# Kernel optimization log

Measured on AMD Instinct MI355X. Metric: run time of the kernel, lower is better.

The kernel has to match this reference:

```python
import jax, jax.numpy as jnp
import numpy as np

B, T, C, H, HS, L, V, BITS = 4, 512, 768, 12, 64, 12, 50257, 16


def _ln(x, g, b, eps=1e-5):
    m = x.mean(-1, keepdims=True)
    v = ((x - m) ** 2).mean(-1, keepdims=True)
    return (x - m) * jax.lax.rsqrt(v + eps) * g + b


def setup_inputs() -> dict:
    key = jax.random.key(0)
    ks = jax.random.split(key, 12)
    s = 0.02
    return {
        "idx": jax.random.randint(ks[0], (B, T), 0, V),
        "tok_emb": jax.random.normal(ks[1], (V, C), jnp.float32) * s,
        "pos_emb": jax.random.normal(ks[2], (T, C), jnp.float32) * s,
        "Wq": jax.random.normal(ks[3], (L, H, C, HS), jnp.float32) * s,
        "Wk": jax.random.normal(ks[4], (L, H, C, HS), jnp.float32) * s,
        "Wv": jax.random.normal(ks[5], (L, H, C, HS), jnp.float32) * s,
        "Wo": jax.random.normal(ks[6], (L, C, C), jnp.float32) * s,
        "bo": jnp.zeros((L, C), jnp.float32),
        "W1": jax.random.normal(ks[7], (L, C, 4 * C), jnp.float32) * s,
        "b1": jnp.zeros((L, 4 * C), jnp.float32),
        "W2": jax.random.normal(ks[8], (L, 4 * C, C), jnp.float32) * s,
        "b2": jnp.zeros((L, C), jnp.float32),
        "ln1_g": jnp.ones((L, C), jnp.float32),
        "ln1_b": jnp.zeros((L, C), jnp.float32),
        "ln2_g": jnp.ones((L, C), jnp.float32),
        "ln2_b": jnp.zeros((L, C), jnp.float32),
        "lnf_g": jnp.ones((C,), jnp.float32),
        "lnf_b": jnp.zeros((C,), jnp.float32),
        "Wh": jax.random.normal(ks[9], (C, BITS), jnp.float32) * s,
        "bh": jnp.zeros((BITS,), jnp.float32),
    }


def reference(idx, tok_emb, pos_emb, Wq, Wk, Wv, Wo, bo, W1, b1, W2, b2,
              ln1_g, ln1_b, ln2_g, ln2_b, lnf_g, lnf_b, Wh, bh):
    Bc, Tc = idx.shape
    x = tok_emb[idx] + pos_emb[:Tc]          # [B,T,C]
    mask = jnp.tril(jnp.ones((Tc, Tc), bool))  # causal tril buffer
    scale = HS ** -0.5

    def block(x, p):
        wq, wk, wv, wo, bo_, w1, b1_, w2, b2_, g1, bb1, g2, bb2 = p
        xn = _ln(x, g1, bb1)
        q = jnp.einsum('btc,hcd->bhtd', xn, wq)
        k = jnp.einsum('btc,hcd->bhtd', xn, wk)
        v = jnp.einsum('btc,hcd->bhtd', xn, wv)
        wei = jnp.einsum('bhtd,bhsd->bhts', q, k) * scale
        wei = jnp.where(mask, wei, -jnp.inf)
        wei = jax.nn.softmax(wei, axis=-1)
        o = jnp.einsum('bhts,bhsd->bhtd', wei, v)
        o = o.transpose(0, 2, 1, 3).reshape(Bc, Tc, H * HS)  # concat heads
        x = x + o @ wo + bo_
        xn2 = _ln(x, g2, bb2)
        h = jax.nn.gelu(xn2 @ w1 + b1_, approximate=False)  # exact GELU (torch default)
        x = x + h @ w2 + b2_
        return x, None

    x, _ = jax.lax.scan(block, x, (Wq, Wk, Wv, Wo, bo, W1, b1, W2, b2,
                                   ln1_g, ln1_b, ln2_g, ln2_b))
    x = _ln(x, lnf_g, lnf_b)
    logits = x @ Wh + bh                      # [B,T,16] ECOC logits
    return logits
```

## Files before the change

### kernel.cpp

```cpp
#include <hip/hip_runtime.h>
#include <hip/hip_bf16.h>
#include <math.h>

#define TT   512
#define CC   768
#define HH   12
#define HSZ  64
#define LL   12
#define C4   3072
#define BTOT 2048
#define NQKV 2304
#define NX   ((long)BTOT * CC)

typedef __attribute__((ext_vector_type(8))) short short8;
typedef __attribute__((ext_vector_type(4))) float f32x4;

__device__ __forceinline__ unsigned short f2b_bits(float f) {
    unsigned u = __float_as_uint(f);
    return (unsigned short)((u + 0x7fffu + ((u >> 16) & 1u)) >> 16);
}
__device__ __forceinline__ float b2f(unsigned short b) {
    return __uint_as_float((unsigned)b << 16);
}
__device__ __forceinline__ float gelu_t(float v) {
    float u = 0.7978845608f * fmaf(0.044715f * v, v * v, v);
    float th = 1.f - 2.f / (1.f + __expf(2.f * u));
    return 0.5f * v * (1.f + th);
}

__device__ __forceinline__ void gl_lds16(const void* g, void* l) {
    __builtin_amdgcn_global_load_lds(
        (const __attribute__((address_space(1))) unsigned int*)g,
        (__attribute__((address_space(3))) unsigned int*)l,
        16, 0, 0);
}

__global__ __launch_bounds__(256) void embed_ln(const int* __restrict__ idx,
    const float* __restrict__ tok, const float* __restrict__ pos,
    const float* __restrict__ g, const float* __restrict__ b,
    float* __restrict__ x, __hip_bfloat16* __restrict__ y)
{
    int r = blockIdx.x, tid = threadIdx.x;
    int t = r & (TT - 1);
    long id = idx[r];
    const float* te = tok + id * (long)CC;
    const float* pe = pos + (long)t * CC;
    float* xr = x + (long)r * CC;
    float v[3];
#pragma unroll
    for (int i = 0; i < 3; ++i) {
        int c = tid + i * 256;
        v[i] = te[c] + pe[c];
        xr[c] = v[i];
    }
    float s  = v[0] + v[1] + v[2];
    float sq = v[0]*v[0] + v[1]*v[1] + v[2]*v[2];
#pragma unroll
    for (int off = 32; off > 0; off >>= 1) {
        s  += __shfl_down(s, off);
        sq += __shfl_down(sq, off);
    }
    __shared__ float ss[4], ssq[4];
    int w = tid >> 6;
    if ((tid & 63) == 0) { ss[w] = s; ssq[w] = sq; }
    __syncthreads();
    s  = ss[0] + ss[1] + ss[2] + ss[3];
    sq = ssq[0] + ssq[1] + ssq[2] + ssq[3];
    float mean = s * (1.0f / CC);
    float var  = sq * (1.0f / CC) - mean * mean;
    float rs   = rsqrtf(var + 1e-5f);
    __hip_bfloat16* yr = y + (long)r * CC;
#pragma unroll
    for (int i = 0; i < 3; ++i) {
        int c = tid + i * 256;
        yr[c] = __float2bfloat16((v[i] - mean) * rs * g[c] + b[c]);
    }
}

template <bool DOLN>
__global__ __launch_bounds__(256) void red_ln(float* __restrict__ x,
    const unsigned short* __restrict__ p, const float* __restrict__ bias,
    const float* __restrict__ g, const float* __restrict__ b,
    __hip_bfloat16* __restrict__ y)
{
    int r = blockIdx.x, tid = threadIdx.x;
    float* xr = x + (long)r * CC;
    const unsigned short* pr = p + (long)r * CC;
    float v[3];
#pragma unroll
    for (int i = 0; i < 3; ++i) {
        int c = tid + i * 256;
        float s = xr[c] + bias[c];
        s += b2f(pr[c]);
        s += b2f(pr[c + 1 * NX]);
        s += b2f(pr[c + 2 * NX]);
        s += b2f(pr[c + 3 * NX]);
        xr[c] = s;
        v[i] = s;
    }
    if (!DOLN) return;
    float s  = v[0] + v[1] + v[2];
    float sq = v[0]*v[0] + v[1]*v[1] + v[2]*v[2];
#pragma unroll
    for (int off = 32; off > 0; off >>= 1) {
        s  += __shfl_down(s, off);
        sq += __shfl_down(sq, off);
    }
    __shared__ float ss[4], ssq[4];
    int w = tid >> 6;
    if ((tid & 63) == 0) { ss[w] = s; ssq[w] = sq; }
    __syncthreads();
    s  = ss[0] + ss[1] + ss[2] + ss[3];
    sq = ssq[0] + ssq[1] + ssq[2] + ssq[3];
    float mean = s * (1.0f / CC);
    float var  = sq * (1.0f / CC) - mean * mean;
    float rs   = rsqrtf(var + 1e-5f);
    __hip_bfloat16* yr = y + (long)r * CC;
#pragma unroll
    for (int i = 0; i < 3; ++i) {
        int c = tid + i * 256;
        yr[c] = __float2bfloat16((v[i] - mean) * rs * g[c] + b[c]);
    }
}

__global__ __launch_bounds__(256) void cvtT_k(const float* __restrict__ src,
    __hip_bfloat16* __restrict__ dst, int R, int D, long sSrc, long sDst)
{
    src += (long)blockIdx.z * sSrc;
    dst += (long)blockIdx.z * sDst;
    __shared__ float t[64][65];
    int d0 = blockIdx.x * 64, r0 = blockIdx.y * 64;
    int tid = threadIdx.x;
#pragma unroll
    for (int i = 0; i < 4; ++i) {
        int flat = tid + i * 256;
        int r = flat >> 4, c4 = (flat & 15) * 4;
        float4 v = *(const float4*)&src[(long)(r0 + r) * D + d0 + c4];
        t[r][c4 + 0] = v.x; t[r][c4 + 1] = v.y;
        t[r][c4 + 2] = v.z; t[r][c4 + 3] = v.w;
    }
    __syncthreads();
#pragma unroll
    for (int i = 0; i < 4; ++i) {
        int flat = tid + i * 256;
        int n = flat >> 4, kq = (flat & 15) * 4;
        ushort4 o;
        o.x = f2b_bits(t[kq + 0][n]); o.y = f2b_bits(t[kq + 1][n]);
        o.z = f2b_bits(t[kq + 2][n]); o.w = f2b_bits(t[kq + 3][n]);
        *(ushort4*)&dst[(long)(d0 + n) * R + r0 + kq] = o;
    }
}

__global__ __launch_bounds__(256) void cvt_qkvT(const float* __restrict__ Wq,
    const float* __restrict__ Wk, const float* __restrict__ Wv,
    __hip_bfloat16* __restrict__ out)
{
    int c0 = blockIdx.x * 64;
    int g  = blockIdx.y;
    int l  = blockIdx.z;
    int which = g / 12, h = g % 12;
    const long wAtt = (long)HH * CC * HSZ;
    const float* src = (which == 0 ? Wq : which == 1 ? Wk : Wv)
                       + l * wAtt + (long)h * CC * HSZ;
    __hip_bfloat16* dst = out + (long)l * NQKV * CC + (long)(which * CC + h * HSZ) * CC;
    __shared__ float t[64][65];
    int tid = threadIdx.x;
#pragma unroll
    for (int i = 0; i < 4; ++i) {
        int flat = tid + i * 256;
        int r = flat >> 4, c4 = (flat & 15) * 4;
        float4 v = *(const float4*)&src[(long)(c0 + r) * HSZ + c4];
        t[r][c4 + 0] = v.x; t[r][c4 + 1] = v.y;
        t[r][c4 + 2] = v.z; t[r][c4 + 3] = v.w;
    }
    __syncthreads();
#pragma unroll
    for (int i = 0; i < 4; ++i) {
        int flat = tid + i * 256;
        int n = flat >> 4, kq = (flat & 15) * 4;
        ushort4 o;
        o.x = f2b_bits(t[kq + 0][n]); o.y = f2b_bits(t[kq + 1][n]);
        o.z = f2b_bits(t[kq + 2][n]); o.w = f2b_bits(t[kq + 3][n]);
        *(ushort4*)&dst[(long)n * CC + c0 + kq] = o;
    }
}

template <int EPI>
__global__ __launch_bounds__(256, 3) void gemm_bf16(
    const __hip_bfloat16* __restrict__ A,
    const __hip_bfloat16* __restrict__ BT,
    __hip_bfloat16* __restrict__ Cb, float* __restrict__ Cf,
    const float* __restrict__ bias, __hip_bfloat16* __restrict__ Vt,
    int K, int lda, int ldb, int ldc)
{
    __shared__ short Asm[4][64 * 32];
    __shared__ short Bsm[4][128 * 32];
    const int tid  = threadIdx.x;
    const int lane = tid & 63;
    const int wid  = tid >> 6;
    const int wm = wid >> 1, wn = wid & 1;

    const int gx = gridDim.x;
    const int slice = gx * gridDim.y;
    int flat = blockIdx.y * gx + blockIdx.x;
    int swz  = (flat & 7) * (slice >> 3) + (flat >> 3);
    const int row0 = (swz / gx) * 64, col0 = (swz % gx) * 128;
    const int sk = (EPI == 5) ? blockIdx.z : 0;

    const int gr = tid >> 2;
    const int cb = ((tid & 3) + (tid >> 3)) & 3;
    const int gk = cb * 8;
    const __hip_bfloat16* Ap = A  + (long)(row0 + gr) * lda + sk * K + gk;
    const __hip_bfloat16* Bp = BT + (long)(col0 + gr) * ldb + sk * K + gk;
    const int lofs = wid * 512;

    f32x4 acc[2][4] = {};
    const int fr = lane & 15, g = lane >> 4;

    int offA[2], offB[4];
#pragma unroll
    for (int m = 0; m < 2; ++m) {
        int row = wm * 32 + m * 16 + fr;
        offA[m] = row * 32 + (((g - (row >> 1)) & 3) * 8);
    }
#pragma unroll
    for (int n = 0; n < 4; ++n) {
        int row = wn * 64 + n * 16 + fr;
        offB[n] = row * 32 + (((g - (row >> 1)) & 3) * 8);
    }

#define STAGE(buf)                                                          \
    do {                                                                    \
        gl_lds16(Ap, &Asm[buf][lofs]);                                      \
        gl_lds16(Bp, &Bsm[buf][lofs]);                                      \
        gl_lds16(Bp + (long)64 * ldb, &Bsm[buf][lofs + 64 * 32]);           \
        Ap += 32; Bp += 32;                                                 \
    } while (0)

    STAGE(0); STAGE(1); STAGE(2);

    const int nt = K >> 5;
    for (int t = 0; t < nt; ++t) {
        if (t < nt - 2)       asm volatile("s_waitcnt vmcnt(6)" ::: "memory");
        else if (t == nt - 2) asm volatile("s_waitcnt vmcnt(3)" ::: "memory");
        else                  asm volatile("s_waitcnt vmcnt(0)" ::: "memory");
        __builtin_amdgcn_s_barrier();
        __builtin_amdgcn_sched_barrier(0);
        if (t + 3 < nt) STAGE((t + 3) & 3);

        const int cur = t & 3;
        short8 af[2], bf[4];
#pragma unroll
        for (int m = 0; m < 2; ++m)
            af[m] = *(const short8*)&Asm[cur][offA[m]];
#pragma unroll
        for (int n = 0; n < 4; ++n)
            bf[n] = *(const short8*)&Bsm[cur][offB[n]];
#pragma unroll
        for (int m = 0; m < 2; ++m)
#pragma unroll
            for (int n = 0; n < 4; ++n)
                acc[m][n] = __builtin_amdgcn_mfma_f32_16x16x32_bf16(
                    af[m], bf[n], acc[m][n], 0, 0, 0);
    }
#undef STAGE

    const int fq = lane >> 4;
#pragma unroll
    for (int m = 0; m < 2; ++m) {
        int rbase = row0 + wm * 32 + m * 16 + fq * 4;
#pragma unroll
        for (int n = 0; n < 4; ++n) {
            int col = col0 + wn * 64 + n * 16 + fr;
            if (EPI == 1 && col >= 1536) {
                int hd = col - 1536;
                int b = rbase >> 9, t = rbase & (TT - 1);
                ushort4 o;
                o.x = f2b_bits(acc[m][n][0]); o.y = f2b_bits(acc[m][n][1]);
                o.z = f2b_bits(acc[m][n][2]); o.w = f2b_bits(acc[m][n][3]);
                *(ushort4*)&Vt[((long)(b * HH + (hd >> 6)) * HSZ + (hd & 63)) * TT + t] = o;
                continue;
            }
            float bv = (EPI == 2) ? bias[col] : 0.f;
#pragma unroll
            for (int j = 0; j < 4; ++j) {
                long row = rbase + j;
                float v = acc[m][n][j];
                if (EPI == 1) {
                    Cb[row * ldc + col] = __float2bfloat16(v);
                } else if (EPI == 2) {
                    Cb[row * ldc + col] = __float2bfloat16(gelu_t(v + bv));
                } else {
                    Cb[(long)sk * NX + row * ldc + col] = __float2bfloat16(v);
                }
            }
        }
    }
}

__global__ __launch_bounds__(64) void attn_mfma(
    const __hip_bfloat16* __restrict__ qkv,
    const __hip_bfloat16* __restrict__ vT,
    __hip_bfloat16* __restrict__ o)
{
    int flat = blockIdx.x + 16 * (blockIdx.y + 12 * blockIdx.z);
    int swz  = (flat & 7) * 96 + (flat >> 3);
    const int qt = swz & 15;
    const int h  = (swz >> 4) % 12;
    const int b  = swz / 192;
    const int lane = threadIdx.x;
    const int t0 = qt * 32;
    const int fr = lane & 15, g = lane >> 4;

    __shared__ unsigned short P_lds[2][32 * 40];
    __shared__ float corr_lds[2][32], l_lds[32];

    const long qbaseA = ((long)(b * TT + t0 + fr)) * NQKV + h * HSZ + g * 8;
    const long qbaseB = qbaseA + (long)16 * NQKV;
    short8 qfA0 = *(const short8*)(qkv + qbaseA);
    short8 qfA1 = *(const short8*)(qkv + qbaseA + 32);
    short8 qfB0 = *(const short8*)(qkv + qbaseB);
    short8 qfB1 = *(const short8*)(qkv + qbaseB + 32);

    f32x4 oaccA[4] = {}, oaccB[4] = {};
    float mA = -3.0e38f, lA = 0.f, mB = -3.0e38f, lB = 0.f;
    const int t_laneA = t0 + fr;
    const int t_laneB = t0 + 16 + fr;
    const int smax = t0 + 31;
    const long kcol = CC + h * HSZ + g * 8;
    const long vrow = (((long)(b * HH + h) * HSZ) + fr) * TT + g * 8;

    short8 ka0, ka1, ka2, ka3;
    {
        long kb0 = ((long)(b * TT + fr)) * NQKV + kcol;
        long kb1 = ((long)(b * TT + 16 + fr)) * NQKV + kcol;
        ka0 = *(const short8*)(qkv + kb0);
        ka1 = *(const short8*)(qkv + kb0 + 32);
        ka2 = *(const short8*)(qkv + kb1);
        ka3 = *(const short8*)(qkv + kb1 + 32);
    }

    for (int s0 = 0; s0 <= smax; s0 += 32) {
        const int pc = (s0 >> 5) & 1;
        f32x4 stA0 = {}, stA1 = {}, stB0 = {}, stB1 = {};
        stA0 = __builtin_amdgcn_mfma_f32_16x16x32_bf16(ka0, qfA0, stA0, 0, 0, 0);
        stA0 = __builtin_amdgcn_mfma_f32_16x16x32_bf16(ka1, qfA1, stA0, 0, 0, 0);
        stA1 = __builtin_amdgcn_mfma_f32_16x16x32_bf16(ka2, qfA0, stA1, 0, 0, 0);
        stA1 = __builtin_amdgcn_mfma_f32_16x16x32_bf16(ka3, qfA1, stA1, 0, 0, 0);
        stB0 = __builtin_amdgcn_mfma_f32_16x16x32_bf16(ka0, qfB0, stB0, 0, 0, 0);
        stB0 = __builtin_amdgcn_mfma_f32_16x16x32_bf16(ka1, qfB1, stB0, 0, 0, 0);
        stB1 = __builtin_amdgcn_mfma_f32_16x16x32_bf16(ka2, qfB0, stB1, 0, 0, 0);
        stB1 = __builtin_amdgcn_mfma_f32_16x16x32_bf16(ka3, qfB1, stB1, 0, 0, 0);

        const bool more = (s0 + 32 <= smax);
        short8 kn0, kn1, kn2, kn3;
        if (more) {
            long kb0 = ((long)(b * TT + s0 + 32 + fr)) * NQKV + kcol;
            long kb1 = ((long)(b * TT + s0 + 48 + fr)) * NQKV + kcol;
            kn0 = *(const short8*)(qkv + kb0);
            kn1 = *(const short8*)(qkv + kb0 + 32);
            kn2 = *(const short8*)(qkv + kb1);
            kn3 = *(const short8*)(qkv + kb1 + 32);
        }
        short8 vc0 = *(const short8*)(vT + vrow + s0);
        short8 vc1 = *(const short8*)(vT + vrow + 16 * TT + s0);
        short8 vc2 = *(const short8*)(vT + vrow + 32 * TT + s0);
        short8 vc3 = *(const short8*)(vT + vrow + 48 * TT + s0);

        float pA[8];
        float mxA = -3.0e38f;
#pragma unroll
        for (int j = 0; j < 4; ++j) {
            int s = s0 + g * 4 + j;
            float v = stA0[j] * 0.125f;
            v = (s <= t_laneA) ? v : -3.0e38f;
            pA[j] = v; mxA = fmaxf(mxA, v);
        }
#pragma unroll
        for (int j = 0; j < 4; ++j) {
            int s = s0 + 16 + g * 4 + j;
            float v = stA1[j] * 0.125f;
            v = (s <= t_laneA) ? v : -3.0e38f;
            pA[4 + j] = v; mxA = fmaxf(mxA, v);
        }
        mxA = fmaxf(mxA, __shfl_xor(mxA, 16));
        mxA = fmaxf(mxA, __shfl_xor(mxA, 32));
        float mnewA = fmaxf(mA, mxA);
        float corrA = __expf(mA - mnewA);
        float psA = 0.f;
#pragma unroll
        for (int i = 0; i < 8; ++i) {
            float e = __expf(pA[i] - mnewA);
            pA[i] = e; psA += e;
        }
        psA += __shfl_xor(psA, 16);
        psA += __shfl_xor(psA, 32);
        lA = lA * corrA + psA;
        mA = mnewA;

        float pB[8];
        float mxB = -3.0e38f;
#pragma unroll
        for (int j = 0; j < 4; ++j) {
            int s = s0 + g * 4 + j;
            float v = stB0[j] * 0.125f;
            v = (s <= t_laneB) ? v : -3.0e38f;
            pB[j] = v; mxB = fmaxf(mxB, v);
        }
#pragma unroll
        for (int j = 0; j < 4; ++j) {
            int s = s0 + 16 + g * 4 + j;
            float v = stB1[j] * 0.125f;
            v = (s <= t_laneB) ? v : -3.0e38f;
            pB[4 + j] = v; mxB = fmaxf(mxB, v);
        }
        mxB = fmaxf(mxB, __shfl_xor(mxB, 16));
        mxB = fmaxf(mxB, __shfl_xor(mxB, 32));
        float mnewB = fmaxf(mB, mxB);
        float corrB = __expf(mB - mnewB);
        float psB = 0.f;
#pragma unroll
        for (int i = 0; i < 8; ++i) {
            float e = __expf(pB[i] - mnewB);
            pB[i] = e; psB += e;
        }
        psB += __shfl_xor(psB, 16);
        psB += __shfl_xor(psB, 32);
        lB = lB * corrB + psB;
        mB = mnewB;

        unsigned short* P_w = &P_lds[pc][0];
        if (lane < 16) { corr_lds[pc][lane] = corrA; corr_lds[pc][16 + lane] = corrB; }
        {
            unsigned u0 = (unsigned)f2b_bits(pA[0]) | ((unsigned)f2b_bits(pA[1]) << 16);
            unsigned u1 = (unsigned)f2b_bits(pA[2]) | ((unsigned)f2b_bits(pA[3]) << 16);
            unsigned u2 = (unsigned)f2b_bits(pA[4]) | ((unsigned)f2b_bits(pA[5]) << 16);
            unsigned u3 = (unsigned)f2b_bits(pA[6]) | ((unsigned)f2b_bits(pA[7]) << 16);
            *(unsigned*)&P_w[fr * 40 + g * 4]          = u0;
            *(unsigned*)&P_w[fr * 40 + g * 4 + 2]      = u1;
            *(unsigned*)&P_w[fr * 40 + 16 + g * 4]     = u2;
            *(unsigned*)&P_w[fr * 40 + 16 + g * 4 + 2] = u3;
        }
        {
            unsigned u0 = (unsigned)f2b_bits(pB[0]) | ((unsigned)f2b_bits(pB[1]) << 16);
            unsigned u1 = (unsigned)f2b_bits(pB[2]) | ((unsigned)f2b_bits(pB[3]) << 16);
            unsigned u2 = (unsigned)f2b_bits(pB[4]) | ((unsigned)f2b_bits(pB[5]) << 16);
            unsigned u3 = (unsigned)f2b_bits(pB[6]) | ((unsigned)f2b_bits(pB[7]) << 16);
            *(unsigned*)&P_w[(16 + fr) * 40 + g * 4]          = u0;
            *(unsigned*)&P_w[(16 + fr) * 40 + g * 4 + 2]      = u1;
            *(unsigned*)&P_w[(16 + fr) * 40 + 16 + g * 4]     = u2;
            *(unsigned*)&P_w[(16 + fr) * 40 + 16 + g * 4 + 2] = u3;
        }
        __builtin_amdgcn_sched_barrier(0);

        float crA0 = corr_lds[pc][g * 4 + 0], crA1 = corr_lds[pc][g * 4 + 1];
        float crA2 = corr_lds[pc][g * 4 + 2], crA3 = corr_lds[pc][g * 4 + 3];
        float crB0 = corr_lds[pc][16 + g * 4 + 0], crB1 = corr_lds[pc][16 + g * 4 + 1];
        float crB2 = corr_lds[pc][16 + g * 4 + 2], crB3 = corr_lds[pc][16 + g * 4 + 3];
        short8 pfA = *(const short8*)&P_w[fr * 40 + g * 8];
        short8 pfB = *(const short8*)&P_w[(16 + fr) * 40 + g * 8];
#pragma unroll
        for (int dt = 0; dt < 4; ++dt) {
            short8 vc = (dt == 0) ? vc0 : (dt == 1) ? vc1 : (dt == 2) ? vc2 : vc3;
            oaccA[dt][0] *= crA0; oaccA[dt][1] *= crA1;
            oaccA[dt][2] *= crA2; oaccA[dt][3] *= crA3;
            oaccA[dt] = __builtin_amdgcn_mfma_f32_16x16x32_bf16(pfA, vc, oaccA[dt], 0, 0, 0);
            oaccB[dt][0] *= crB0; oaccB[dt][1] *= crB1;
            oaccB[dt][2] *= crB2; oaccB[dt][3] *= crB3;
            oaccB[dt] = __builtin_amdgcn_mfma_f32_16x16x32_bf16(pfB, vc, oaccB[dt], 0, 0, 0);
        }

        if (more) { ka0 = kn0; ka1 = kn1; ka2 = kn2; ka3 = kn3; }
    }

    if (lane < 16) { l_lds[lane] = lA; l_lds[16 + lane] = lB; }
    __builtin_amdgcn_sched_barrier(0);
    float ilA0 = 1.f / l_lds[g * 4 + 0], ilA1 = 1.f / l_lds[g * 4 + 1];
    float ilA2 = 1.f / l_lds[g * 4 + 2], ilA3 = 1.f / l_lds[g * 4 + 3];
    float ilB0 = 1.f / l_lds[16 + g * 4 + 0], ilB1 = 1.f / l_lds[16 + g * 4 + 1];
    float ilB2 = 1.f / l_lds[16 + g * 4 + 2], ilB3 = 1.f / l_lds[16 + g * 4 + 3];
#pragma unroll
    for (int dt = 0; dt < 4; ++dt) {
        long cbaseA = (long)(b * TT + t0) * CC + h * HSZ + dt * 16 + fr;
        long cbaseB = cbaseA + (long)16 * CC;
        o[cbaseA + (g * 4 + 0) * (long)CC] = __float2bfloat16(oaccA[dt][0] * ilA0);
        o[cbaseA + (g * 4 + 1) * (long)CC] = __float2bfloat16(oaccA[dt][1] * ilA1);
        o[cbaseA + (g * 4 + 2) * (long)CC] = __float2bfloat16(oaccA[dt][2] * ilA2);
        o[cbaseA + (g * 4 + 3) * (long)CC] = __float2bfloat16(oaccA[dt][3] * ilA3);
        o[cbaseB + (g * 4 + 0) * (long)CC] = __float2bfloat16(oaccB[dt][0] * ilB0);
        o[cbaseB + (g * 4 + 1) * (long)CC] = __float2bfloat16(oaccB[dt][1] * ilB1);
        o[cbaseB + (g * 4 + 2) * (long)CC] = __float2bfloat16(oaccB[dt][2] * ilB2);
        o[cbaseB + (g * 4 + 3) * (long)CC] = __float2bfloat16(oaccB[dt][3] * ilB3);
    }
}

__global__ __launch_bounds__(256) void head_bf(const __hip_bfloat16* __restrict__ xn,
    const float* __restrict__ Wh, const float* __restrict__ bh,
    float* __restrict__ out)
{
    int r = blockIdx.x, tid = threadIdx.x;
    const unsigned short* xr = (const unsigned short*)(xn + (long)r * CC);
    float acc[16];
#pragma unroll
    for (int j = 0; j < 16; ++j) acc[j] = 0.f;
#pragma unroll
    for (int i = 0; i < 3; ++i) {
        int c = tid + i * 256;
        float xnv = b2f(xr[c]);
        const float* wr = Wh + (long)c * 16;
#pragma unroll
        for (int j = 0; j < 16; ++j) acc[j] = fmaf(xnv, wr[j], acc[j]);
    }
#pragma unroll
    for (int off = 32; off > 0; off >>= 1)
#pragma unroll
        for (int j = 0; j < 16; ++j) acc[j] += __shfl_down(acc[j], off);
    __shared__ float red[4][16];
    int w = tid >> 6;
    if ((tid & 63) == 0)
#pragma unroll
        for (int j = 0; j < 16; ++j) red[w][j] = acc[j];
    __syncthreads();
    if (tid < 16)
        out[(long)r * 16 + tid] =
            red[0][tid] + red[1][tid] + red[2][tid] + red[3][tid] + bh[tid];
}

extern "C" void kernel_launch(void* const* d_in, const int* in_sizes, int n_in,
                              void* d_out, int out_size, void* d_ws, size_t ws_size,
                              hipStream_t stream)
{
    const int*   idx  = (const int*)  d_in[0];
    const float* tok  = (const float*)d_in[1];
    const float* pos  = (const float*)d_in[2];
    const float* Wq   = (const float*)d_in[3];
    const float* Wk   = (const float*)d_in[4];
    const float* Wv   = (const float*)d_in[5];
    const float* Wo   = (const float*)d_in[6];
    const float* bo   = (const float*)d_in[7];
    const float* W1   = (const float*)d_in[8];
    const float* b1   = (const float*)d_in[9];
    const float* W2   = (const float*)d_in[10];
    const float* b2   = (const float*)d_in[11];
    const float* ln1g = (const float*)d_in[12];
    const float* ln1b = (const float*)d_in[13];
    const float* ln2g = (const float*)d_in[14];
    const float* ln2b = (const float*)d_in[15];
    const float* lnfg = (const float*)d_in[16];
    const float* lnfb = (const float*)d_in[17];
    const float* Wh   = (const float*)d_in[18];
    const float* bh   = (const float*)d_in[19];

    char* w = (char*)d_ws;
    float*          x     = (float*)w;          w += NX * 4;
    __hip_bfloat16* xn_b  = (__hip_bfloat16*)w; w += NX * 2;
    __hip_bfloat16* qkvb  = (__hip_bfloat16*)w; w += (long)BTOT * NQKV * 2;
    __hip_bfloat16* vT    = (__hip_bfloat16*)w; w += NX * 2;
    __hip_bfloat16* o_b   = (__hip_bfloat16*)w; w += NX * 2;
    __hip_bfloat16* hb    = (__hip_bfloat16*)w; w += (long)BTOT * C4 * 2;
    __hip_bfloat16* qkvT  = (__hip_bfloat16*)w; w += (long)LL * NQKV * CC * 2;
    __hip_bfloat16* woT   = (__hip_bfloat16*)w; w += (long)LL * CC * CC * 2;
    __hip_bfloat16* w1T   = (__hip_bfloat16*)w; w += (long)LL * C4 * CC * 2;
    __hip_bfloat16* w2T   = (__hip_bfloat16*)w; w += (long)LL * CC * C4 * 2;
    __hip_bfloat16* pbuf  = (__hip_bfloat16*)w; w += 4 * NX * 2;

    cvt_qkvT<<<dim3(12, 36, LL), 256, 0, stream>>>(Wq, Wk, Wv, qkvT);
    cvtT_k<<<dim3(12, 12, LL), 256, 0, stream>>>(Wo, woT, CC, CC,
        (long)CC * CC, (long)CC * CC);
    cvtT_k<<<dim3(48, 12, LL), 256, 0, stream>>>(W1, w1T, CC, C4,
        (long)CC * C4, (long)CC * C4);
    cvtT_k<<<dim3(12, 48, LL), 256, 0, stream>>>(W2, w2T, C4, CC,
        (long)C4 * CC, (long)C4 * CC);

    embed_ln<<<BTOT, 256, 0, stream>>>(idx, tok, pos, ln1g, ln1b, x, xn_b);

    for (int l = 0; l < LL; ++l) {
        gemm_bf16<1><<<dim3(NQKV / 128, BTOT / 64), 256, 0, stream>>>(
            xn_b, qkvT + (long)l * NQKV * CC, qkvb, nullptr, nullptr, vT,
            CC, CC, CC, NQKV);

        attn_mfma<<<dim3(TT / 32, HH, 4), 64, 0, stream>>>(qkvb, vT, o_b);

        gemm_bf16<5><<<dim3(CC / 128, BTOT / 64, 4), 256, 0, stream>>>(
            o_b, woT + (long)l * CC * CC, pbuf, nullptr, nullptr, nullptr,
            192, CC, CC, CC);

        red_ln<true><<<BTOT, 256, 0, stream>>>(x, (const unsigned short*)pbuf,
            bo + l * CC, ln2g + l * CC, ln2b + l * CC, xn_b);

        gemm_bf16<2><<<dim3(C4 / 128, BTOT / 64), 256, 0, stream>>>(
            xn_b, w1T + (long)l * C4 * CC, hb, nullptr, b1 + l * C4, nullptr,
            CC, CC, CC, C4);

        gemm_bf16<5><<<dim3(CC / 128, BTOT / 64, 4), 256, 0, stream>>>(
            hb, w2T + (long)l * CC * C4, pbuf, nullptr, nullptr, nullptr,
            768, C4, C4, CC);

        const float* gN = (l < LL - 1) ? (ln1g + (l + 1) * CC) : lnfg;
        const float* bN = (l < LL - 1) ? (ln1b + (l + 1) * CC) : lnfb;
        red_ln<true><<<BTOT, 256, 0, stream>>>(x, (const unsigned short*)pbuf,
            b2 + l * CC, gN, bN, xn_b);
    }

    head_bf<<<BTOT, 256, 0, stream>>>(xn_b, Wh, bh, (float*)d_out);
}
```

Baseline: 1.370 ms.

## Fuse split-K reduction and LayerNorm into GEMM via last-block atomic counter

Removes the separate red_ln kernels after the Wo and W2 split-K GEMMs. Each GEMM block increments a per-row-slab atomic counter, and the last block to finish a 64-row slab sums the four partial buffers, adds the bias and residual, and applies LayerNorm. This saves two kernel launches per layer and one pass over the partials, at the cost of a serialized tail where a single block per slab handles 64 rows x 768 columns. The diff also removes the red_ln definition, and the embed_ln body is edited so that its LN tail now attaches to it.

Measured after the change: 3.075 ms. 2.24x slower.

```diff
diff --git a/kernel.cpp b/kernel.cpp
--- a/kernel.cpp
+++ b/kernel.cpp
@@ -53,52 +53,6 @@
         v[i] = te[c] + pe[c];
         xr[c] = v[i];
     }
-    float s  = v[0] + v[1] + v[2];
-    float sq = v[0]*v[0] + v[1]*v[1] + v[2]*v[2];
-#pragma unroll
-    for (int off = 32; off > 0; off >>= 1) {
-        s  += __shfl_down(s, off);
-        sq += __shfl_down(sq, off);
-    }
-    __shared__ float ss[4], ssq[4];
-    int w = tid >> 6;
-    if ((tid & 63) == 0) { ss[w] = s; ssq[w] = sq; }
-    __syncthreads();
-    s  = ss[0] + ss[1] + ss[2] + ss[3];
-    sq = ssq[0] + ssq[1] + ssq[2] + ssq[3];
-    float mean = s * (1.0f / CC);
-    float var  = sq * (1.0f / CC) - mean * mean;
-    float rs   = rsqrtf(var + 1e-5f);
-    __hip_bfloat16* yr = y + (long)r * CC;
-#pragma unroll
-    for (int i = 0; i < 3; ++i) {
-        int c = tid + i * 256;
-        yr[c] = __float2bfloat16((v[i] - mean) * rs * g[c] + b[c]);
-    }
-}
-
-template <bool DOLN>
-__global__ __launch_bounds__(256) void red_ln(float* __restrict__ x,
-    const unsigned short* __restrict__ p, const float* __restrict__ bias,
-    const float* __restrict__ g, const float* __restrict__ b,
-    __hip_bfloat16* __restrict__ y)
-{
-    int r = blockIdx.x, tid = threadIdx.x;
-    float* xr = x + (long)r * CC;
-    const unsigned short* pr = p + (long)r * CC;
-    float v[3];
-#pragma unroll
-    for (int i = 0; i < 3; ++i) {
-        int c = tid + i * 256;
-        float s = xr[c] + bias[c];
-        s += b2f(pr[c]);
-        s += b2f(pr[c + 1 * NX]);
-        s += b2f(pr[c + 2 * NX]);
-        s += b2f(pr[c + 3 * NX]);
-        xr[c] = s;
-        v[i] = s;
-    }
-    if (!DOLN) return;
     float s  = v[0] + v[1] + v[2];
     float sq = v[0]*v[0] + v[1]*v[1] + v[2]*v[2];
 #pragma unroll
@@ -189,8 +143,10 @@
 __global__ __launch_bounds__(256, 3) void gemm_bf16(
     const __hip_bfloat16* __restrict__ A,
     const __hip_bfloat16* __restrict__ BT,
-    __hip_bfloat16* __restrict__ Cb, float* __restrict__ Cf,
+    __hip_bfloat16* __restrict__ Cb, float* __restrict__ xR,
     const float* __restrict__ bias, __hip_bfloat16* __restrict__ Vt,
+    const float* __restrict__ gln, const float* __restrict__ bln,
+    int* __restrict__ cnt,
     int K, int lda, int ldb, int ldc)
 {
     __shared__ short Asm[4][64 * 32];
@@ -205,7 +161,7 @@
     int flat = blockIdx.y * gx + blockIdx.x;
     int swz  = (flat & 7) * (slice >> 3) + (flat >> 3);
     const int row0 = (swz / gx) * 64, col0 = (swz % gx) * 128;
-    const int sk = (EPI == 5) ? blockIdx.z : 0;
+    const int sk = (EPI == 6) ? blockIdx.z : 0;
 
     const int gr = tid >> 2;
     const int cb = ((tid & 3) + (tid >> 3)) & 3;
@@ -294,6 +250,63 @@
                     Cb[(long)sk * NX + row * ldc + col] = __float2bfloat16(v);
                 }
             }
+        }
+    }
+
+    if (EPI != 6) return;
+
+    __shared__ int isLast;
+    __syncthreads();
+    if (tid == 0) {
+        __threadfence();
+        const int slab = row0 >> 6;
+        const int nC = gx * gridDim.z;
+        int old = __hip_atomic_fetch_add(&cnt[slab], 1,
+                      __ATOMIC_ACQ_REL, __HIP_MEMORY_SCOPE_AGENT);
+        int last = (old == nC - 1);
+        if (last)
+            __hip_atomic_store(&cnt[slab], 0,
+                __ATOMIC_RELAXED, __HIP_MEMORY_SCOPE_AGENT);
+        isLast = last;
+    }
+    __syncthreads();
+    if (!isLast) return;
+    __threadfence();
+
+    const unsigned short* pb = (const unsigned short*)Cb;
+    const int w4 = tid >> 6;
+#pragma unroll 1
+    for (int rr = 0; rr < 16; ++rr) {
+        int r = (row0) + w4 * 16 + rr;
+        float* xr = xR + (long)r * CC;
+        const unsigned short* pr = pb + (long)r * CC;
+        float vv[12];
+        float s = 0.f, sq = 0.f;
+#pragma unroll
+        for (int i = 0; i < 12; ++i) {
+            int c = lane + i * 64;
+            float t = xr[c] + bias[c];
+            t += b2f(pr[c]);
+            t += b2f(pr[c + 1 * NX]);
+            t += b2f(pr[c + 2 * NX]);
+            t += b2f(pr[c + 3 * NX]);
+            xr[c] = t;
+            vv[i] = t;
+            s += t; sq += t * t;
+        }
+#pragma unroll
+        for (int off = 32; off > 0; off >>= 1) {
+            s  += __shfl_xor(s, off);
+            sq += __shfl_xor(sq, off);
+        }
+        float mean = s * (1.0f / CC);
+        float var  = sq * (1.0f / CC) - mean * mean;
+        float rs   = rsqrtf(var + 1e-5f);
+        __hip_bfloat16* yr = Vt + (long)r * CC;
+#pragma unroll
+        for (int i = 0; i < 12; ++i) {
+            int c = lane + i * 64;
+            yr[c] = __float2bfloat16((vv[i] - mean) * rs * gln[c] + bln[c]);
         }
     }
 }
@@ -563,6 +576,9 @@
     __hip_bfloat16* w1T   = (__hip_bfloat16*)w; w += (long)LL * C4 * CC * 2;
     __hip_bfloat16* w2T   = (__hip_bfloat16*)w; w += (long)LL * CC * C4 * 2;
     __hip_bfloat16* pbuf  = (__hip_bfloat16*)w; w += 4 * NX * 2;
+    int*            cnt   = (int*)w;            w += 128;
+
+    hipMemsetAsync(cnt, 0, 32 * sizeof(int), stream);
 
     cvt_qkvT<<<dim3(12, 36, LL), 256, 0, stream>>>(Wq, Wk, Wv, qkvT);
     cvtT_k<<<dim3(12, 12, LL), 256, 0, stream>>>(Wo, woT, CC, CC,
@@ -577,29 +593,23 @@
     for (int l = 0; l < LL; ++l) {
         gemm_bf16<1><<<dim3(NQKV / 128, BTOT / 64), 256, 0, stream>>>(
             xn_b, qkvT + (long)l * NQKV * CC, qkvb, nullptr, nullptr, vT,
-            CC, CC, CC, NQKV);
+            nullptr, nullptr, nullptr, CC, CC, CC, NQKV);
 
         attn_mfma<<<dim3(TT / 32, HH, 4), 64, 0, stream>>>(qkvb, vT, o_b);
 
-        gemm_bf16<5><<<dim3(CC / 128, BTOT / 64, 4), 256, 0, stream>>>(
-            o_b, woT + (long)l * CC * CC, pbuf, nullptr, nullptr, nullptr,
-            192, CC, CC, CC);
-
-        red_ln<true><<<BTOT, 256, 0, stream>>>(x, (const unsigned short*)pbuf,
-            bo + l * CC, ln2g + l * CC, ln2b + l * CC, xn_b);
+        gemm_bf16<6><<<dim3(CC / 128, BTOT / 64, 4), 256, 0, stream>>>(
+            o_b, woT + (long)l * CC * CC, pbuf, x, bo + l * CC, xn_b,
+            ln2g + l * CC, ln2b + l * CC, cnt, 192, CC, CC, CC);
 
         gemm_bf16<2><<<dim3(C4 / 128, BTOT / 64), 256, 0, stream>>>(
             xn_b, w1T + (long)l * C4 * CC, hb, nullptr, b1 + l * C4, nullptr,
-            CC, CC, CC, C4);
-
-        gemm_bf16<5><<<dim3(CC / 128, BTOT / 64, 4), 256, 0, stream>>>(
-            hb, w2T + (long)l * CC * C4, pbuf, nullptr, nullptr, nullptr,
-            768, C4, C4, CC);
+            nullptr, nullptr, nullptr, CC, CC, CC, C4);
 
         const float* gN = (l < LL - 1) ? (ln1g + (l + 1) * CC) : lnfg;
         const float* bN = (l < LL - 1) ? (ln1b + (l + 1) * CC) : lnfb;
-        red_ln<true><<<BTOT, 256, 0, stream>>>(x, (const unsigned short*)pbuf,
-            b2 + l * CC, gN, bN, xn_b);
+        gemm_bf16<6><<<dim3(CC / 128, BTOT / 64, 4), 256, 0, stream>>>(
+            hb, w2T + (long)l * CC * C4, pbuf, x, b2 + l * CC, xn_b,
+            gN, bN, cnt, 768, C4, C4, CC);
     }
 
     head_bf<<<BTOT, 256, 0, stream>>>(xn_b, Wh, bh, (float*)d_out);
```
